# Performance work log

Measured on AMD Instinct MI355X. Metric: run time of the kernel, lower is better.

## Reference

```python
import jax, jax.numpy as jnp
import numpy as np

BETA = 0.5  # exp-sum normalization exponent (not a true softmax)


def setup_inputs() -> dict:
    key = jax.random.key(0)
    ks = jax.random.split(key, 12)
    b, h = 1024, 200
    item_num, region_num, user_num = 50000, 1000, 10000
    d, hid = 128, 128  # embed_size == hidden_size (required by the bmm reshape)
    std = 0.01
    return {
        "history": jax.random.randint(ks[0], (1, b, h), 0, item_num),
        "target": jax.random.randint(ks[1], (1, b), 0, item_num),
        "history_region": jax.random.randint(ks[2], (1, b, h), 0, region_num),
        "target_region": jax.random.randint(ks[3], (1, b), 0, region_num),
        "history_visit_rate": jax.random.uniform(ks[4], (1, h), dtype=jnp.float32),
        "dist_mat": jax.random.uniform(ks[5], (b, h), dtype=jnp.float32),
        "uid": 7,
        "embed_target": std * jax.random.normal(ks[6], (item_num, d // 2), dtype=jnp.float32),
        "embed_region": std * jax.random.normal(ks[7], (region_num, d // 2), dtype=jnp.float32),
        "embed_dist": std * jax.random.normal(ks[8], (user_num, region_num), dtype=jnp.float32),
        "Wq": jax.random.normal(ks[9], (hid, d), dtype=jnp.float32) * (1.0 / np.sqrt(d)),
        "Wk": jax.random.normal(ks[10], (hid, d), dtype=jnp.float32) * (1.0 / np.sqrt(d)),
        "Wv": jax.random.normal(ks[11], (d, d), dtype=jnp.float32) * (1.0 / np.sqrt(d)),
    }


def reference(history, target, history_region, target_region, history_visit_rate,
              dist_mat, uid, embed_target, embed_region, embed_dist, Wq, Wk, Wv):
    h_idx = history[0]            # [b, h]
    tgt = target[0]               # [b]
    hr = history_region[0]        # [b, h]
    tr = target_region[0]         # [b]
    hv = history_visit_rate[0]    # [h]
    b, hlen = h_idx.shape

    # embedding gathers + concat (target half | region half)
    hist_emb = jnp.concatenate([embed_target[h_idx], embed_region[hr]], axis=-1)  # [b,h,d]
    tgt_emb = jnp.concatenate([embed_target[tgt], embed_region[tr]], axis=-1)     # [b,d]
    hd = embed_dist[uid][hr]      # [b, h]
    td = embed_dist[uid][tr]      # [b]
    d = tgt_emb.shape[1]

    # QKV projections (torch Linear: y = x @ W.T)
    q = tgt_emb @ Wq.T            # [b, d]  (hidden == d)
    k = hist_emb @ Wk.T           # [b, h, d]
    v = hist_emb @ Wv.T           # [b, h, d]

    # faithful to original: key reshaped (NOT transposed) to [b, d, h]
    k_r = k.reshape(b, d, hlen)
    scores = jnp.einsum('bd,bdh->bh', q, k_r) / jnp.sqrt(jnp.float32(d))  # [b,h]

    # exp / beta-normalized attention with equality mask
    mask = (h_idx != tgt[:, None]).astype(scores.dtype)
    exp_A = jnp.exp(scores) * mask                          # [b,h]
    exp_sum = jnp.sum(exp_A, axis=-1) ** BETA               # [b]
    attn = exp_A / exp_sum[:, None]                         # [b,h]

    # geo weights: td @ hd is a vector-matrix product -> [h], broadcast over b
    geo = jnp.exp(-1.0 / (jax.nn.relu(td @ hd) + 1.0) * dist_mat)  # [b,h]

    result1 = v * (attn + geo)[..., None]                   # [b,h,d]
    result2 = hist_emb * jnp.broadcast_to(hv, (b, hlen))[..., None]
    result = result1 + result2                              # [b,h,d]

    pred = jnp.einsum('bhd,bd->b', result, tgt_emb)         # bmm + sum over h
    return jax.nn.sigmoid(pred)
```

## Files before the change

### kernel.cpp

```cpp
#include <hip/hip_runtime.h>

typedef unsigned short USH;
typedef unsigned int   UIN;
typedef unsigned char  UCH;

static constexpr int Bn = 1024;
static constexpr int Hn = 200;
static constexpr int Dn = 128;
static constexpr int Dh = 64;
static constexpr int NITEM = 50000;
static constexpr int NREG  = 1000;
static constexpr int MT = 64;
static constexpr int AB_A_BLOCKS = (NITEM + MT - 1) / MT;
static constexpr int AB_B_BLOCKS = (NREG  + MT - 1) / MT;
static constexpr int AB_TOT = AB_A_BLOCKS + AB_B_BLOCKS;
static constexpr int QU_BLOCKS = Bn / 4;
static constexpr int G_BLOCKS  = Bn / 16;
static constexpr int WTS = 132;
static constexpr int ETS = 69;
static constexpr int CR  = 50;

static constexpr float FSCALE = 128.f;
static constexpr float FINV   = 1.f / 128.f;

__device__ __forceinline__ float bf2f(USH u) {
  return __uint_as_float(((UIN)u) << 16);
}
__device__ __forceinline__ USH f2b(float f) {
  UIN x = __float_as_uint(f);
  return (USH)((x + 0x7fffu + ((x >> 16) & 1u)) >> 16);
}
__device__ __forceinline__ UIN enc4(float a, float b, float c, float d) {
  int w = __builtin_amdgcn_cvt_pk_fp8_f32(a, b, 0, false);
  w = __builtin_amdgcn_cvt_pk_fp8_f32(c, d, w, true);
  return (UIN)w;
}
__device__ __forceinline__ void dec4(UIN w, float* o) {
  auto lo = __builtin_amdgcn_cvt_pk_f32_fp8((int)w, false);
  auto hi = __builtin_amdgcn_cvt_pk_f32_fp8((int)w, true);
  o[0] = lo[0]; o[1] = lo[1]; o[2] = hi[0]; o[3] = hi[1];
}

__global__ __launch_bounds__(256, 2) void ab_kernel(
    const float* __restrict__ Et, const float* __restrict__ Er,
    const float* __restrict__ Wk, const float* __restrict__ Wq,
    const float* __restrict__ Wv, const int* __restrict__ target,
    const int* __restrict__ tregion, const int* __restrict__ hregion,
    const float* __restrict__ embed_dist, const int* __restrict__ uid,
    UCH* __restrict__ Ap, UCH* __restrict__ Bp,
    UCH* __restrict__ Ar, UCH* __restrict__ Br,
    float* __restrict__ qvt, float* __restrict__ uvt, float* __restrict__ g) {
  __shared__ float wt[64 * WTS];
  __shared__ float et[MT * ETS];
  int blk = blockIdx.x, tid = threadIdx.x;

  if (blk >= AB_TOT + QU_BLOCKS) {
    int c = tid;
    const float* row = embed_dist + (size_t)uid[0] * NREG;
    float acc = 0.f;
    int ibase = (blk - AB_TOT - QU_BLOCKS) * 16;
    for (int ii = 0; ii < 16; ii++) {
      int i = ibase + ii;
      float td = row[tregion[i]];
      if (c < Hn) acc += td * row[hregion[(size_t)i * Hn + c]];
    }
    if (c < Hn) atomicAdd(&g[c], acc);
    return;
  }

  if (blk >= AB_TOT) {
    float* te = wt;
    int i0 = (blk - AB_TOT) * 4;
#pragma unroll
    for (int v = 0; v < 2; v++) {
      int idx = v * 256 + tid;
      int ii = idx >> 7, d = idx & 127;
      int it = i0 + ii;
      te[ii * 128 + d] = (d < 64) ? Et[(size_t)target[it] * Dh + d]
                                  : Er[(size_t)tregion[it] * Dh + (d - 64)];
    }
    __syncthreads();
    int j = tid & 127, half = tid >> 7;
    float a0 = 0.f, a1 = 0.f, a2 = 0.f, a3 = 0.f;
    if (half == 0) {
      const float* wr = Wq + (size_t)j * Dn;
#pragma unroll 8
      for (int k = 0; k < 128; k++) {
        float w = wr[k];
        a0 += w * te[k]; a1 += w * te[128 + k];
        a2 += w * te[256 + k]; a3 += w * te[384 + k];
      }
      const float s = 0.088388347648318447f;
      qvt[(size_t)(i0 + 0) * Dn + j] = a0 * s;
      qvt[(size_t)(i0 + 1) * Dn + j] = a1 * s;
      qvt[(size_t)(i0 + 2) * Dn + j] = a2 * s;
      qvt[(size_t)(i0 + 3) * Dn + j] = a3 * s;
    } else {
      int d = j;
#pragma unroll 8
      for (int k = 0; k < 128; k++) {
        float w = Wv[(size_t)k * Dn + d];
        a0 += w * te[k]; a1 += w * te[128 + k];
        a2 += w * te[256 + k]; a3 += w * te[384 + k];
      }
      uvt[(size_t)(i0 + 0) * Dn + d] = a0;
      uvt[(size_t)(i0 + 1) * Dn + d] = a1;
      uvt[(size_t)(i0 + 2) * Dn + d] = a2;
      uvt[(size_t)(i0 + 3) * Dn + d] = a3;
    }
    return;
  }

  const float* E; UCH* OutP; UCH* OutR; int nmax, base, koff;
  if (blk < AB_A_BLOCKS) { E = Et; OutP = Ap; OutR = Ar; nmax = NITEM; base = blk * MT; koff = 0; }
  else { E = Er; OutP = Bp; OutR = Br; nmax = NREG; base = (blk - AB_A_BLOCKS) * MT; koff = 64; }

#pragma unroll
  for (int p = 0; p < 8; p++) {
    int idx = p * 256 + tid;
    int row = idx >> 4, c4 = idx & 15;
    float4 w = *reinterpret_cast<const float4*>(Wk + (size_t)row * Dn + koff + c4 * 4);
    wt[(c4 * 4 + 0) * WTS + row] = w.x;
    wt[(c4 * 4 + 1) * WTS + row] = w.y;
    wt[(c4 * 4 + 2) * WTS + row] = w.z;
    wt[(c4 * 4 + 3) * WTS + row] = w.w;
  }
#pragma unroll
  for (int p = 0; p < 4; p++) {
    int idx = p * 256 + tid;
    int m = idx >> 4, c4 = idx & 15;
    int gi = base + m;
    float4 e = make_float4(0.f, 0.f, 0.f, 0.f);
    if (gi < nmax) e = *reinterpret_cast<const float4*>(E + (size_t)gi * Dh + c4 * 4);
    et[m * ETS + c4 * 4 + 0] = e.x;
    et[m * ETS + c4 * 4 + 1] = e.y;
    et[m * ETS + c4 * 4 + 2] = e.z;
    et[m * ETS + c4 * 4 + 3] = e.w;
  }
  __syncthreads();

#pragma unroll
  for (int p = 0; p < 4; p++) {
    int idx = p * 256 + tid;
    int m = idx >> 4, wr = idx & 15;
    int gi = base + m;
    if (gi < nmax) {
      const float* er = &et[m * ETS + wr * 4];
      *reinterpret_cast<UIN*>(OutR + (size_t)gi * 64 + wr * 4) =
          enc4(er[0] * FSCALE, er[1] * FSCALE, er[2] * FSCALE, er[3] * FSCALE);
    }
  }

  int jt = tid & 15, it = tid >> 4;
  const float* wb = wt + jt * 8;
  const float* eb = et + (it * 4) * ETS;
  float c[4][8];
#pragma unroll
  for (int ii = 0; ii < 4; ii++)
#pragma unroll
    for (int jj = 0; jj < 8; jj++) c[ii][jj] = 0.f;

#pragma unroll 2
  for (int k = 0; k < 64; k++) {
    float4 w0 = *reinterpret_cast<const float4*>(wb + (size_t)k * WTS);
    float4 w1 = *reinterpret_cast<const float4*>(wb + (size_t)k * WTS + 4);
    float e0 = eb[k], e1 = eb[ETS + k], e2 = eb[2 * ETS + k], e3 = eb[3 * ETS + k];
    c[0][0] += e0 * w0.x; c[0][1] += e0 * w0.y; c[0][2] += e0 * w0.z; c[0][3] += e0 * w0.w;
    c[0][4] += e0 * w1.x; c[0][5] += e0 * w1.y; c[0][6] += e0 * w1.z; c[0][7] += e0 * w1.w;
    c[1][0] += e1 * w0.x; c[1][1] += e1 * w0.y; c[1][2] += e1 * w0.z; c[1][3] += e1 * w0.w;
    c[1][4] += e1 * w1.x; c[1][5] += e1 * w1.y; c[1][6] += e1 * w1.z; c[1][7] += e1 * w1.w;
    c[2][0] += e2 * w0.x; c[2][1] += e2 * w0.y; c[2][2] += e2 * w0.z; c[2][3] += e2 * w0.w;
    c[2][4] += e2 * w1.x; c[2][5] += e2 * w1.y; c[2][6] += e2 * w1.z; c[2][7] += e2 * w1.w;
    c[3][0] += e3 * w0.x; c[3][1] += e3 * w0.y; c[3][2] += e3 * w0.z; c[3][3] += e3 * w0.w;
    c[3][4] += e3 * w1.x; c[3][5] += e3 * w1.y; c[3][6] += e3 * w1.z; c[3][7] += e3 * w1.w;
  }

#pragma unroll
  for (int ii = 0; ii < 4; ii++) {
    int item = base + it * 4 + ii;
    if (item < nmax) {
      uint2 pk;
      pk.x = enc4(c[ii][0] * FSCALE, c[ii][1] * FSCALE, c[ii][2] * FSCALE, c[ii][3] * FSCALE);
      pk.y = enc4(c[ii][4] * FSCALE, c[ii][5] * FSCALE, c[ii][6] * FSCALE, c[ii][7] * FSCALE);
      *reinterpret_cast<uint2*>(OutP + (size_t)item * 128 + jt * 8) = pk;
    }
  }
}

__global__ __launch_bounds__(256, 6) void sc_kernel(
    const int* __restrict__ history, const int* __restrict__ target,
    const int* __restrict__ hregion, const int* __restrict__ tregion,
    const float* __restrict__ Et, const float* __restrict__ Er,
    const float* __restrict__ qvt, const float* __restrict__ uvt,
    const UCH* __restrict__ Ap, const UCH* __restrict__ Bp,
    const UCH* __restrict__ Ar, const UCH* __restrict__ Br,
    float* __restrict__ psc, float2* __restrict__ s12) {
  __shared__ USH kvs[CR * Dn];
  __shared__ float tgtE[128], uvf[128], qv[32];
  int b = blockIdx.x, i = b >> 2, h = b & 3;
  int tid = threadIdx.x;
  const int* hrow = history + (size_t)i * Hn + CR * h;
  const int* rrow = hregion + (size_t)i * Hn + CR * h;

  if (tid < 128) {
    tgtE[tid] = FINV * ((tid < 64) ? Et[(size_t)target[i] * Dh + tid]
                                   : Er[(size_t)tregion[i] * Dh + (tid - 64)]);
  } else {
    uvf[tid - 128] = FINV * uvt[(size_t)i * Dn + (tid - 128)];
  }
  if (tid < 32) qv[tid] = FINV * qvt[(size_t)i * Dn + 32 * h + tid];

  {
    int rlane = tid & 15, rgrp = tid >> 4;
#pragma unroll
    for (int p = 0; p < 4; p++) {
      int t = p * 16 + rgrp;
      if (t < CR) {
        int ia = hrow[t], ib = rrow[t];
        uint2 av = *reinterpret_cast<const uint2*>(Ap + (size_t)ia * 128 + rlane * 8);
        uint2 bv = *reinterpret_cast<const uint2*>(Bp + (size_t)ib * 128 + rlane * 8);
        float fa[8], fb[8];
        dec4(av.x, fa); dec4(av.y, fa + 4);
        dec4(bv.x, fb); dec4(bv.y, fb + 4);
        uint4 pk;
        pk.x = (UIN)f2b(fa[0] + fb[0]) | ((UIN)f2b(fa[1] + fb[1]) << 16);
        pk.y = (UIN)f2b(fa[2] + fb[2]) | ((UIN)f2b(fa[3] + fb[3]) << 16);
        pk.z = (UIN)f2b(fa[4] + fb[4]) | ((UIN)f2b(fa[5] + fb[5]) << 16);
        pk.w = (UIN)f2b(fa[6] + fb[6]) | ((UIN)f2b(fa[7] + fb[7]) << 16);
        *reinterpret_cast<uint4*>(&kvs[t * Dn + rlane * 8]) = pk;
      }
    }
  }

  int l8 = tid & 7, r8 = tid >> 3;
  int ta = r8, tb = 32 + r8;
  bool hasb = (tb < CR);
  uint2 ea, ra, eb2, rb2;
  {
    int iaa = hrow[ta], iba = rrow[ta];
    ea = *reinterpret_cast<const uint2*>(Ar + (size_t)iaa * 64 + l8 * 8);
    ra = *reinterpret_cast<const uint2*>(Br + (size_t)iba * 64 + l8 * 8);
    if (hasb) {
      int iab = hrow[tb], ibb = rrow[tb];
      eb2 = *reinterpret_cast<const uint2*>(Ar + (size_t)iab * 64 + l8 * 8);
      rb2 = *reinterpret_cast<const uint2*>(Br + (size_t)ibb * 64 + l8 * 8);
    }
  }
  __syncthreads();

#pragma unroll
  for (int pass = 0; pass < 2; pass++) {
    if (pass == 1 && !hasb) break;
    uint2 e = (pass == 0) ? ea : eb2;
    uint2 r = (pass == 0) ? ra : rb2;
    int t = (pass == 0) ? ta : tb;
    float fe[8], fr[8];
    dec4(e.x, fe); dec4(e.y, fe + 4);
    dec4(r.x, fr); dec4(r.y, fr + 4);
    const float* u0 = &uvf[l8 * 8];       const float* t0 = &tgtE[l8 * 8];
    const float* u1 = &uvf[64 + l8 * 8];  const float* t1 = &tgtE[64 + l8 * 8];
    float s1a = fe[0] * u0[0] + fe[1] * u0[1] + fe[2] * u0[2] + fe[3] * u0[3]
              + fe[4] * u0[4] + fe[5] * u0[5] + fe[6] * u0[6] + fe[7] * u0[7]
              + fr[0] * u1[0] + fr[1] * u1[1] + fr[2] * u1[2] + fr[3] * u1[3]
              + fr[4] * u1[4] + fr[5] * u1[5] + fr[6] * u1[6] + fr[7] * u1[7];
    float s2a = fe[0] * t0[0] + fe[1] * t0[1] + fe[2] * t0[2] + fe[3] * t0[3]
              + fe[4] * t0[4] + fe[5] * t0[5] + fe[6] * t0[6] + fe[7] * t0[7]
              + fr[0] * t1[0] + fr[1] * t1[1] + fr[2] * t1[2] + fr[3] * t1[3]
              + fr[4] * t1[4] + fr[5] * t1[5] + fr[6] * t1[6] + fr[7] * t1[7];
    s1a += __shfl_xor(s1a, 1, 64); s2a += __shfl_xor(s2a, 1, 64);
    s1a += __shfl_xor(s1a, 2, 64); s2a += __shfl_xor(s2a, 2, 64);
    s1a += __shfl_xor(s1a, 4, 64); s2a += __shfl_xor(s2a, 4, 64);
    if (l8 == 0) s12[(size_t)i * Hn + CR * h + t] = make_float2(s1a, s2a);
  }

  if (tid < Hn) {
    float acc = 0.f;
    const USH* kp = &kvs[tid];
#pragma unroll
    for (int a = 0; a < 32; a++) acc += qv[a] * bf2f(kp[a * 200]);
    psc[((size_t)i * 4 + h) * Hn + tid] = acc;
  }
}

__global__ __launch_bounds__(256, 8) void ep_kernel(
    const int* __restrict__ history, const int* __restrict__ target,
    const float* __restrict__ hv, const float* __restrict__ dist_mat,
    const float* __restrict__ g, const float* __restrict__ psc,
    const float2* __restrict__ s12, float* __restrict__ out) {
  __shared__ float red[8];
  int i = blockIdx.x, tid = threadIdx.x, lane = tid & 63, wave = tid >> 6;
  int tgt_i = target[i];

  float ea = 0.f; float2 sv = make_float2(0.f, 0.f);
  if (tid < Hn) {
    const float* pp = psc + (size_t)i * 4 * Hn + tid;
    float s = (pp[0] + pp[Hn]) + (pp[2 * Hn] + pp[3 * Hn]);
    sv = s12[(size_t)i * Hn + tid];
    ea = (history[(size_t)i * Hn + tid] != tgt_i) ? __expf(s) : 0.f;
  }
  float wsum = ea;
  for (int off = 32; off > 0; off >>= 1) wsum += __shfl_down(wsum, off, 64);
  if (lane == 0) red[wave] = wsum;
  __syncthreads();
  float esum = red[0] + red[1] + red[2] + red[3];
  float inv = esum > 0.f ? 1.f / sqrtf(esum) : 0.f;

  float part = 0.f;
  if (tid < Hn) {
    float gc = g[tid]; gc = gc > 0.f ? gc : 0.f;
    float dm = dist_mat[(size_t)i * Hn + tid];
    float geo = __expf(-dm / (gc + 1.f));
    part = (ea * inv + geo) * sv.x + hv[tid] * sv.y;
  }
  __syncthreads();
  for (int off = 32; off > 0; off >>= 1) part += __shfl_down(part, off, 64);
  if (lane == 0) red[wave] = part;
  __syncthreads();
  if (tid == 0) {
    float pred = red[0] + red[1] + red[2] + red[3];
    out[i] = 1.f / (1.f + __expf(-pred));
  }
}

extern "C" void kernel_launch(void* const* d_in, const int* in_sizes, int n_in,
                              void* d_out, int out_size, void* d_ws, size_t ws_size,
                              hipStream_t stream) {
  const int*   history = (const int*)d_in[0];
  const int*   target  = (const int*)d_in[1];
  const int*   hregion = (const int*)d_in[2];
  const int*   tregion = (const int*)d_in[3];
  const float* hv      = (const float*)d_in[4];
  const float* dist    = (const float*)d_in[5];
  const int*   uid     = (const int*)d_in[6];
  const float* Et      = (const float*)d_in[7];
  const float* Er      = (const float*)d_in[8];
  const float* Edist   = (const float*)d_in[9];
  const float* Wq      = (const float*)d_in[10];
  const float* Wk      = (const float*)d_in[11];
  const float* Wv      = (const float*)d_in[12];

  char* w = (char*)d_ws;
  float* g   = (float*)w;
  UCH*   Ap  = (UCH*)(w + 1024);
  UCH*   Bp  = Ap + (size_t)NITEM * 128;
  UCH*   Ar  = Bp + (size_t)NREG * 128;
  UCH*   Br  = Ar + (size_t)NITEM * 64;
  float* qvt = (float*)(Br + (size_t)NREG * 64);
  float* uvt = qvt + (size_t)Bn * Dn;
  float* psc = uvt + (size_t)Bn * Dn;
  float2* s12 = (float2*)(psc + (size_t)Bn * 4 * Hn);
  float* out = (float*)d_out;

  hipMemsetAsync(g, 0, Hn * sizeof(float), stream);
  ab_kernel<<<AB_TOT + QU_BLOCKS + G_BLOCKS, 256, 0, stream>>>(
      Et, Er, Wk, Wq, Wv, target, tregion, hregion, Edist, uid,
      Ap, Bp, Ar, Br, qvt, uvt, g);
  sc_kernel<<<Bn * 4, 256, 0, stream>>>(history, target, hregion, tregion,
                                        Et, Er, qvt, uvt, Ap, Bp, Ar, Br, psc, s12);
  ep_kernel<<<Bn, 256, 0, stream>>>(history, target, hv, dist, g, psc, s12, out);
}
```

Baseline: 153.3 us.

## Interleave projected and raw fp8 embedding rows into one 192-byte record

Merges the separate fp8 tables for projected keys (128 B) and raw embeddings (64 B) into a single 192-byte row per item and per region, so each gathered row in the score kernel touches one contiguous region instead of two. The score kernel now loads the raw halves with 16-byte vector loads into shared staging buffers and reads them from there for the dot products. The key-projection gather also switches to 16-byte loads with 8 threads per row. This trades extra shared memory, which may lower occupancy, for fewer and wider scattered global reads.

```diff
diff --git a/kernel.cpp b/kernel.cpp
--- a/kernel.cpp
+++ b/kernel.cpp
@@ -19,6 +19,7 @@
 static constexpr int WTS = 132;
 static constexpr int ETS = 69;
 static constexpr int CR  = 50;
+static constexpr int RS  = 192;
 
 static constexpr float FSCALE = 128.f;
 static constexpr float FINV   = 1.f / 128.f;
@@ -47,8 +48,7 @@
     const float* __restrict__ Wv, const int* __restrict__ target,
     const int* __restrict__ tregion, const int* __restrict__ hregion,
     const float* __restrict__ embed_dist, const int* __restrict__ uid,
-    UCH* __restrict__ Ap, UCH* __restrict__ Bp,
-    UCH* __restrict__ Ar, UCH* __restrict__ Br,
+    UCH* __restrict__ Cf, UCH* __restrict__ Df,
     float* __restrict__ qvt, float* __restrict__ uvt, float* __restrict__ g) {
   __shared__ float wt[64 * WTS];
   __shared__ float et[MT * ETS];
@@ -111,9 +111,9 @@
     return;
   }
 
-  const float* E; UCH* OutP; UCH* OutR; int nmax, base, koff;
-  if (blk < AB_A_BLOCKS) { E = Et; OutP = Ap; OutR = Ar; nmax = NITEM; base = blk * MT; koff = 0; }
-  else { E = Er; OutP = Bp; OutR = Br; nmax = NREG; base = (blk - AB_A_BLOCKS) * MT; koff = 64; }
+  const float* E; UCH* OutT; int nmax, base, koff;
+  if (blk < AB_A_BLOCKS) { E = Et; OutT = Cf; nmax = NITEM; base = blk * MT; koff = 0; }
+  else { E = Er; OutT = Df; nmax = NREG; base = (blk - AB_A_BLOCKS) * MT; koff = 64; }
 
 #pragma unroll
   for (int p = 0; p < 8; p++) {
@@ -146,7 +146,7 @@
     int gi = base + m;
     if (gi < nmax) {
       const float* er = &et[m * ETS + wr * 4];
-      *reinterpret_cast<UIN*>(OutR + (size_t)gi * 64 + wr * 4) =
+      *reinterpret_cast<UIN*>(OutT + (size_t)gi * RS + 128 + wr * 4) =
           enc4(er[0] * FSCALE, er[1] * FSCALE, er[2] * FSCALE, er[3] * FSCALE);
     }
   }
@@ -182,7 +182,7 @@
       uint2 pk;
       pk.x = enc4(c[ii][0] * FSCALE, c[ii][1] * FSCALE, c[ii][2] * FSCALE, c[ii][3] * FSCALE);
       pk.y = enc4(c[ii][4] * FSCALE, c[ii][5] * FSCALE, c[ii][6] * FSCALE, c[ii][7] * FSCALE);
-      *reinterpret_cast<uint2*>(OutP + (size_t)item * 128 + jt * 8) = pk;
+      *reinterpret_cast<uint2*>(OutT + (size_t)item * RS + jt * 8) = pk;
     }
   }
 }
@@ -192,10 +192,11 @@
     const int* __restrict__ hregion, const int* __restrict__ tregion,
     const float* __restrict__ Et, const float* __restrict__ Er,
     const float* __restrict__ qvt, const float* __restrict__ uvt,
-    const UCH* __restrict__ Ap, const UCH* __restrict__ Bp,
-    const UCH* __restrict__ Ar, const UCH* __restrict__ Br,
+    const UCH* __restrict__ Cf, const UCH* __restrict__ Df,
     float* __restrict__ psc, float2* __restrict__ s12) {
   __shared__ USH kvs[CR * Dn];
+  __shared__ uint4 rawA[CR * 4];
+  __shared__ uint4 rawB[CR * 4];
   __shared__ float tgtE[128], uvf[128], qv[32];
   int b = blockIdx.x, i = b >> 2, h = b & 3;
   int tid = threadIdx.x;
@@ -211,66 +212,65 @@
   if (tid < 32) qv[tid] = FINV * qvt[(size_t)i * Dn + 32 * h + tid];
 
   {
-    int rlane = tid & 15, rgrp = tid >> 4;
-#pragma unroll
-    for (int p = 0; p < 4; p++) {
-      int t = p * 16 + rgrp;
-      if (t < CR) {
-        int ia = hrow[t], ib = rrow[t];
-        uint2 av = *reinterpret_cast<const uint2*>(Ap + (size_t)ia * 128 + rlane * 8);
-        uint2 bv = *reinterpret_cast<const uint2*>(Bp + (size_t)ib * 128 + rlane * 8);
-        float fa[8], fb[8];
-        dec4(av.x, fa); dec4(av.y, fa + 4);
-        dec4(bv.x, fb); dec4(bv.y, fb + 4);
-        uint4 pk;
-        pk.x = (UIN)f2b(fa[0] + fb[0]) | ((UIN)f2b(fa[1] + fb[1]) << 16);
-        pk.y = (UIN)f2b(fa[2] + fb[2]) | ((UIN)f2b(fa[3] + fb[3]) << 16);
-        pk.z = (UIN)f2b(fa[4] + fb[4]) | ((UIN)f2b(fa[5] + fb[5]) << 16);
-        pk.w = (UIN)f2b(fa[6] + fb[6]) | ((UIN)f2b(fa[7] + fb[7]) << 16);
-        *reinterpret_cast<uint4*>(&kvs[t * Dn + rlane * 8]) = pk;
-      }
-    }
-  }
+    int seg = tid & 3, row = tid >> 2;
+    if (row < CR) {
+      int ia = hrow[row], ib = rrow[row];
+      rawA[row * 4 + seg] = *reinterpret_cast<const uint4*>(Cf + (size_t)ia * RS + 128 + seg * 16);
+      rawB[row * 4 + seg] = *reinterpret_cast<const uint4*>(Df + (size_t)ib * RS + 128 + seg * 16);
+    }
+  }
+
+#pragma unroll
+  for (int p = 0; p < 2; p++) {
+    int idx = p * 256 + tid;
+    int seg = idx & 7, row = idx >> 3;
+    if (row < CR) {
+      int ia = hrow[row], ib = rrow[row];
+      uint4 av = *reinterpret_cast<const uint4*>(Cf + (size_t)ia * RS + seg * 16);
+      uint4 bv = *reinterpret_cast<const uint4*>(Df + (size_t)ib * RS + seg * 16);
+      float fa[16], fb[16];
+      dec4(av.x, fa);      dec4(av.y, fa + 4);  dec4(av.z, fa + 8);  dec4(av.w, fa + 12);
+      dec4(bv.x, fb);      dec4(bv.y, fb + 4);  dec4(bv.z, fb + 8);  dec4(bv.w, fb + 12);
+      uint4 k0, k1;
+      k0.x = (UIN)f2b(fa[0] + fb[0])  | ((UIN)f2b(fa[1] + fb[1]) << 16);
+      k0.y = (UIN)f2b(fa[2] + fb[2])  | ((UIN)f2b(fa[3] + fb[3]) << 16);
+      k0.z = (UIN)f2b(fa[4] + fb[4])  | ((UIN)f2b(fa[5] + fb[5]) << 16);
+      k0.w = (UIN)f2b(fa[6] + fb[6])  | ((UIN)f2b(fa[7] + fb[7]) << 16);
+      k1.x = (UIN)f2b(fa[8] + fb[8])  | ((UIN)f2b(fa[9] + fb[9]) << 16);
+      k1.y = (UIN)f2b(fa[10] + fb[10]) | ((UIN)f2b(fa[11] + fb[11]) << 16);
+      k1.z = (UIN)f2b(fa[12] + fb[12]) | ((UIN)f2b(fa[13] + fb[13]) << 16);
+      k1.w = (UIN)f2b(fa[14] + fb[14]) | ((UIN)f2b(fa[15] + fb[15]) << 16);
+      *reinterpret_cast<uint4*>(&kvs[row * Dn + seg * 16]) = k0;
+      *reinterpret_cast<uint4*>(&kvs[row * Dn + seg * 16 + 8]) = k1;
+    }
+  }
+  __syncthreads();
 
   int l8 = tid & 7, r8 = tid >> 3;
-  int ta = r8, tb = 32 + r8;
-  bool hasb = (tb < CR);
-  uint2 ea, ra, eb2, rb2;
-  {
-    int iaa = hrow[ta], iba = rrow[ta];
-    ea = *reinterpret_cast<const uint2*>(Ar + (size_t)iaa * 64 + l8 * 8);
-    ra = *reinterpret_cast<const uint2*>(Br + (size_t)iba * 64 + l8 * 8);
-    if (hasb) {
-      int iab = hrow[tb], ibb = rrow[tb];
-      eb2 = *reinterpret_cast<const uint2*>(Ar + (size_t)iab * 64 + l8 * 8);
-      rb2 = *reinterpret_cast<const uint2*>(Br + (size_t)ibb * 64 + l8 * 8);
-    }
-  }
-  __syncthreads();
-
 #pragma unroll
   for (int pass = 0; pass < 2; pass++) {
-    if (pass == 1 && !hasb) break;
-    uint2 e = (pass == 0) ? ea : eb2;
-    uint2 r = (pass == 0) ? ra : rb2;
-    int t = (pass == 0) ? ta : tb;
-    float fe[8], fr[8];
-    dec4(e.x, fe); dec4(e.y, fe + 4);
-    dec4(r.x, fr); dec4(r.y, fr + 4);
-    const float* u0 = &uvf[l8 * 8];       const float* t0 = &tgtE[l8 * 8];
-    const float* u1 = &uvf[64 + l8 * 8];  const float* t1 = &tgtE[64 + l8 * 8];
-    float s1a = fe[0] * u0[0] + fe[1] * u0[1] + fe[2] * u0[2] + fe[3] * u0[3]
-              + fe[4] * u0[4] + fe[5] * u0[5] + fe[6] * u0[6] + fe[7] * u0[7]
-              + fr[0] * u1[0] + fr[1] * u1[1] + fr[2] * u1[2] + fr[3] * u1[3]
-              + fr[4] * u1[4] + fr[5] * u1[5] + fr[6] * u1[6] + fr[7] * u1[7];
-    float s2a = fe[0] * t0[0] + fe[1] * t0[1] + fe[2] * t0[2] + fe[3] * t0[3]
-              + fe[4] * t0[4] + fe[5] * t0[5] + fe[6] * t0[6] + fe[7] * t0[7]
-              + fr[0] * t1[0] + fr[1] * t1[1] + fr[2] * t1[2] + fr[3] * t1[3]
-              + fr[4] * t1[4] + fr[5] * t1[5] + fr[6] * t1[6] + fr[7] * t1[7];
-    s1a += __shfl_xor(s1a, 1, 64); s2a += __shfl_xor(s2a, 1, 64);
-    s1a += __shfl_xor(s1a, 2, 64); s2a += __shfl_xor(s2a, 2, 64);
-    s1a += __shfl_xor(s1a, 4, 64); s2a += __shfl_xor(s2a, 4, 64);
-    if (l8 == 0) s12[(size_t)i * Hn + CR * h + t] = make_float2(s1a, s2a);
+    int t = (pass == 0) ? r8 : 32 + r8;
+    if (t < CR) {
+      uint2 e = *(reinterpret_cast<const uint2*>(&rawA[t * 4]) + l8);
+      uint2 r = *(reinterpret_cast<const uint2*>(&rawB[t * 4]) + l8);
+      float fe[8], fr[8];
+      dec4(e.x, fe); dec4(e.y, fe + 4);
+      dec4(r.x, fr); dec4(r.y, fr + 4);
+      const float* u0 = &uvf[l8 * 8];       const float* t0 = &tgtE[l8 * 8];
+      const float* u1 = &uvf[64 + l8 * 8];  const float* t1 = &tgtE[64 + l8 * 8];
+      float s1a = fe[0] * u0[0] + fe[1] * u0[1] + fe[2] * u0[2] + fe[3] * u0[3]
+                + fe[4] * u0[4] + fe[5] * u0[5] + fe[6] * u0[6] + fe[7] * u0[7]
+                + fr[0] * u1[0] + fr[1] * u1[1] + fr[2] * u1[2] + fr[3] * u1[3]
+                + fr[4] * u1[4] + fr[5] * u1[5] + fr[6] * u1[6] + fr[7] * u1[7];
+      float s2a = fe[0] * t0[0] + fe[1] * t0[1] + fe[2] * t0[2] + fe[3] * t0[3]
+                + fe[4] * t0[4] + fe[5] * t0[5] + fe[6] * t0[6] + fe[7] * t0[7]
+                + fr[0] * t1[0] + fr[1] * t1[1] + fr[2] * t1[2] + fr[3] * t1[3]
+                + fr[4] * t1[4] + fr[5] * t1[5] + fr[6] * t1[6] + fr[7] * t1[7];
+      s1a += __shfl_xor(s1a, 1, 64); s2a += __shfl_xor(s2a, 1, 64);
+      s1a += __shfl_xor(s1a, 2, 64); s2a += __shfl_xor(s2a, 2, 64);
+      s1a += __shfl_xor(s1a, 4, 64); s2a += __shfl_xor(s2a, 4, 64);
+      if (l8 == 0) s12[(size_t)i * Hn + CR * h + t] = make_float2(s1a, s2a);
+    }
   }
 
   if (tid < Hn) {
@@ -341,11 +341,9 @@
 
   char* w = (char*)d_ws;
   float* g   = (float*)w;
-  UCH*   Ap  = (UCH*)(w + 1024);
-  UCH*   Bp  = Ap + (size_t)NITEM * 128;
-  UCH*   Ar  = Bp + (size_t)NREG * 128;
-  UCH*   Br  = Ar + (size_t)NITEM * 64;
-  float* qvt = (float*)(Br + (size_t)NREG * 64);
+  UCH*   Cf  = (UCH*)(w + 1024);
+  UCH*   Df  = Cf + (size_t)NITEM * RS;
+  float* qvt = (float*)(Df + (size_t)NREG * RS);
   float* uvt = qvt + (size_t)Bn * Dn;
   float* psc = uvt + (size_t)Bn * Dn;
   float2* s12 = (float2*)(psc + (size_t)Bn * 4 * Hn);
@@ -354,8 +352,8 @@
   hipMemsetAsync(g, 0, Hn * sizeof(float), stream);
   ab_kernel<<<AB_TOT + QU_BLOCKS + G_BLOCKS, 256, 0, stream>>>(
       Et, Er, Wk, Wq, Wv, target, tregion, hregion, Edist, uid,
-      Ap, Bp, Ar, Br, qvt, uvt, g);
+      Cf, Df, qvt, uvt, g);
   sc_kernel<<<Bn * 4, 256, 0, stream>>>(history, target, hregion, tregion,
-                                        Et, Er, qvt, uvt, Ap, Bp, Ar, Br, psc, s12);
+                                        Et, Er, qvt, uvt, Cf, Df, psc, s12);
   ep_kernel<<<Bn, 256, 0, stream>>>(history, target, hv, dist, g, psc, s12, out);
 }
```

New measurement: 152.2 us. About the same (-0.7%).
